# Kernel tuning notes

Hardware: AMD Instinct MI355X
Metric: run time of the kernel (lower is better)

The kernel has to match this reference:

```python
import jax, jax.numpy as jnp
import numpy as np

D_MODEL = 1024
NUM_HEADS = 16
D_K = D_MODEL // NUM_HEADS
NEG = jnp.float32(-1e9)  # finite stand-in for -inf to keep softmax NaN-free on fully masked rows


def setup_inputs() -> dict:
    key = jax.random.key(0)
    ks = jax.random.split(key, 7)
    B, N_q, N_kv = 2, 2048, 2048
    x = jax.random.normal(ks[0], (B, N_q, D_MODEL), dtype=jnp.float32)
    K = jax.random.normal(ks[1], (B, NUM_HEADS, N_kv, D_K), dtype=jnp.float32)
    V = jax.random.normal(ks[2], (B, NUM_HEADS, N_kv, D_K), dtype=jnp.float32)
    # pad masks: True = keep. Ensure first kv position is always valid.
    kv_pad_mask = jax.random.uniform(ks[3], (B, 1, 1, N_kv)) > 0.1
    kv_pad_mask = kv_pad_mask.at[..., 0].set(True)
    q_pad_mask = jax.random.uniform(ks[4], (B, 1, N_q, 1)) > 0.1
    # params (torch Linear, bias=False); stored as [in, out] so y = x @ W
    Wq = jax.random.normal(ks[5], (D_MODEL, D_MODEL), dtype=jnp.float32) / np.sqrt(D_MODEL)
    Wo = jax.random.normal(ks[6], (D_MODEL, D_MODEL), dtype=jnp.float32) / np.sqrt(D_MODEL)
    return {"x": x, "K": K, "V": V, "Wq": Wq, "Wo": Wo,
            "kv_pad_mask": kv_pad_mask, "q_pad_mask": q_pad_mask}


def reference(x, K, V, Wq, Wo, kv_pad_mask, q_pad_mask):
    B, N_q, D = x.shape
    H, d_k = NUM_HEADS, D_K
    # Q projection and split into heads: [B, H, N_q, d_k]
    Q = (x @ Wq).reshape(B, N_q, H, d_k).transpose(0, 2, 1, 3)
    scores = jnp.einsum('bhqd,bhkd->bhqk', Q, K) / np.sqrt(d_k).astype(np.float32)
    keep = q_pad_mask & kv_pad_mask  # broadcast to [B,1,N_q,N_kv]
    scores = jnp.where(keep, scores, NEG)
    probs = jax.nn.softmax(scores, axis=-1)
    attn = jnp.einsum('bhqk,bhkd->bhqd', probs, V)  # [B,H,N_q,d_k]
    attn = attn.transpose(0, 2, 1, 3).reshape(B, N_q, H * d_k)
    return attn @ Wo
```

## Files before the change

kernel.cpp:

```cpp
#include <hip/hip_runtime.h>
#include <hip/hip_bf16.h>
#include <stdint.h>

typedef __hip_bfloat16 bf16;
typedef __attribute__((ext_vector_type(8))) short short8;
typedef __attribute__((ext_vector_type(4))) short s16x4;
typedef __attribute__((ext_vector_type(4))) float floatx4;

#define MFMA16(a, b, c) __builtin_amdgcn_mfma_f32_16x16x32_bf16(a, b, c, 0, 0, 0)

__device__ __forceinline__ void async_lds16(const void* g, void* l) {
  __builtin_amdgcn_global_load_lds((__attribute__((address_space(1))) const void*)g,
                                   (__attribute__((address_space(3))) void*)l, 16, 0, 0);
}

__device__ __forceinline__ unsigned rne2(float a, float b) {
  unsigned ua = __float_as_uint(a), ub = __float_as_uint(b);
  ua = ua + 0x7FFFu + ((ua >> 16) & 1u);
  ub = ub + 0x7FFFu + ((ub >> 16) & 1u);
  return (ua >> 16) | (ub & 0xFFFF0000u);
}

__global__ void prep_masks_k(const int* __restrict__ kv, const int* __restrict__ q,
                             float* __restrict__ kvB, float* __restrict__ qB) {
  int i = blockIdx.x * 256 + threadIdx.x;
  kvB[i] = kv[i] ? 0.0f : -3000.0f;
  qB[i]  = q[i]  ? 0.0f : -3000.0f;
}

__global__ void cvt2_k(const float* __restrict__ a, bf16* __restrict__ da,
                       const float* __restrict__ b, bf16* __restrict__ db) {
  int gid = blockIdx.x;
  const float* s; bf16* d;
  if (gid < 4096) { s = a; d = da; } else { s = b; d = db; gid -= 4096; }
  int i = (gid * 256 + threadIdx.x) * 4;
  float4 v = *(const float4*)(s + i);
  uint2 o = {rne2(v.x, v.y), rne2(v.z, v.w)};
  *(uint2*)(d + i) = o;
}

__global__ __launch_bounds__(256) void cvt_transpose_k(const float* __restrict__ src,
                                                       bf16* __restrict__ dst, int R, int C) {
  __shared__ float tile[64][65];
  int m = blockIdx.z;
  int r0 = blockIdx.x * 64, c0 = blockIdx.y * 64;
  const float* s = src + (size_t)m * R * C;
  bf16* d = dst + (size_t)m * R * C;
  int t = threadIdx.x;
  int tr = t >> 2, tg = t & 3;
#pragma unroll
  for (int k = 0; k < 4; ++k) {
    int col = tg * 16 + k * 4;
    float4 v = *(const float4*)(s + (size_t)(r0 + tr) * C + c0 + col);
    tile[tr][col] = v.x; tile[tr][col + 1] = v.y; tile[tr][col + 2] = v.z; tile[tr][col + 3] = v.w;
  }
  __syncthreads();
  int orow = t >> 2, ch = t & 3;
  bf16* drow = d + (size_t)(c0 + orow) * R + r0;
  uint4 w0, w1;
  w0.x = rne2(tile[ch * 8 + 0][orow], tile[ch * 8 + 1][orow]);
  w0.y = rne2(tile[ch * 8 + 2][orow], tile[ch * 8 + 3][orow]);
  w0.z = rne2(tile[ch * 8 + 4][orow], tile[ch * 8 + 5][orow]);
  w0.w = rne2(tile[ch * 8 + 6][orow], tile[ch * 8 + 7][orow]);
  w1.x = rne2(tile[32 + ch * 8 + 0][orow], tile[32 + ch * 8 + 1][orow]);
  w1.y = rne2(tile[32 + ch * 8 + 2][orow], tile[32 + ch * 8 + 3][orow]);
  w1.z = rne2(tile[32 + ch * 8 + 4][orow], tile[32 + ch * 8 + 5][orow]);
  w1.w = rne2(tile[32 + ch * 8 + 6][orow], tile[32 + ch * 8 + 7][orow]);
  *(uint4*)(drow + ch * 8) = w0;
  *(uint4*)(drow + 32 + ch * 8) = w1;
}

__global__ __launch_bounds__(256) void cvtT_w_k(const float* __restrict__ w0p, bf16* __restrict__ d0,
                                                const float* __restrict__ w1p, bf16* __restrict__ d1) {
  __shared__ float tile[64][65];
  const float* s = blockIdx.z ? w1p : w0p;
  bf16* d = blockIdx.z ? d1 : d0;
  int r0 = blockIdx.x * 64, c0 = blockIdx.y * 64;
  int t = threadIdx.x;
  int tr = t >> 2, tg = t & 3;
#pragma unroll
  for (int k = 0; k < 4; ++k) {
    int col = tg * 16 + k * 4;
    float4 v = *(const float4*)(s + (size_t)(r0 + tr) * 1024 + c0 + col);
    tile[tr][col] = v.x; tile[tr][col + 1] = v.y; tile[tr][col + 2] = v.z; tile[tr][col + 3] = v.w;
  }
  __syncthreads();
  int orow = t >> 2, ch = t & 3;
  bf16* drow = d + (size_t)(c0 + orow) * 1024 + r0;
  uint4 a, b;
  a.x = rne2(tile[ch * 8 + 0][orow], tile[ch * 8 + 1][orow]);
  a.y = rne2(tile[ch * 8 + 2][orow], tile[ch * 8 + 3][orow]);
  a.z = rne2(tile[ch * 8 + 4][orow], tile[ch * 8 + 5][orow]);
  a.w = rne2(tile[ch * 8 + 6][orow], tile[ch * 8 + 7][orow]);
  b.x = rne2(tile[32 + ch * 8 + 0][orow], tile[32 + ch * 8 + 1][orow]);
  b.y = rne2(tile[32 + ch * 8 + 2][orow], tile[32 + ch * 8 + 3][orow]);
  b.z = rne2(tile[32 + ch * 8 + 4][orow], tile[32 + ch * 8 + 5][orow]);
  b.w = rne2(tile[32 + ch * 8 + 6][orow], tile[32 + ch * 8 + 7][orow]);
  *(uint4*)(drow + ch * 8) = a;
  *(uint4*)(drow + 32 + ch * 8) = b;
}

__device__ __forceinline__ void storeC(bf16* C, size_t i, float v) { C[i] = __float2bfloat16(v); }
__device__ __forceinline__ void storeC(float* C, size_t i, float v) { C[i] = v; }

template <typename OT>
__global__ __launch_bounds__(256) void gemm_bt_k(const bf16* __restrict__ A,
                                                 const bf16* __restrict__ BT,
                                                 OT* __restrict__ C,
                                                 int M, int N, int K, float scale) {
  __shared__ __align__(16) bf16 As[128 * 64];
  __shared__ __align__(16) bf16 Bs[64 * 64];
  int tid = threadIdx.x;
  int wave = tid >> 6, lane = tid & 63;
  int quad = lane >> 4, lm = lane & 15;
  int wm = wave >> 1, wn = wave & 1;
  int row0 = blockIdx.y * 128, col0 = blockIdx.x * 64;

  floatx4 acc[4][2];
#pragma unroll
  for (int mt = 0; mt < 4; ++mt)
#pragma unroll
    for (int nt = 0; nt < 2; ++nt) acc[mt][nt] = (floatx4){0.f, 0.f, 0.f, 0.f};

  for (int k0 = 0; k0 < K; k0 += 64) {
    __syncthreads();
#pragma unroll
    for (int ch = 0; ch < 4; ++ch) {
      int e = (wave * 4 + ch) * 512 + lane * 8;
      async_lds16(A + (size_t)(row0 + (e >> 6)) * K + k0 + (e & 63), &As[(wave * 4 + ch) * 512]);
    }
#pragma unroll
    for (int ch = 0; ch < 2; ++ch) {
      int e = (wave * 2 + ch) * 512 + lane * 8;
      async_lds16(BT + (size_t)(col0 + (e >> 6)) * K + k0 + (e & 63), &Bs[(wave * 2 + ch) * 512]);
    }
    __syncthreads();
#pragma unroll
    for (int ks = 0; ks < 64; ks += 32) {
      short8 af[4], bfr[2];
#pragma unroll
      for (int mt = 0; mt < 4; ++mt)
        af[mt] = *(const short8*)&As[(wm * 64 + mt * 16 + lm) * 64 + ks + quad * 8];
#pragma unroll
      for (int nt = 0; nt < 2; ++nt)
        bfr[nt] = *(const short8*)&Bs[(wn * 32 + nt * 16 + lm) * 64 + ks + quad * 8];
#pragma unroll
      for (int mt = 0; mt < 4; ++mt)
#pragma unroll
        for (int nt = 0; nt < 2; ++nt)
          acc[mt][nt] = MFMA16(af[mt], bfr[nt], acc[mt][nt]);
    }
  }
#pragma unroll
  for (int mt = 0; mt < 4; ++mt)
#pragma unroll
    for (int nt = 0; nt < 2; ++nt)
#pragma unroll
      for (int j = 0; j < 4; ++j) {
        int rr = row0 + wm * 64 + mt * 16 + quad * 4 + j;
        int cc = col0 + wn * 32 + nt * 16 + lm;
        storeC(C, (size_t)rr * N + cc, acc[mt][nt][j] * scale);
      }
}

__global__ __launch_bounds__(256, 4) void attn_k(const bf16* __restrict__ Q,
                                                 const bf16* __restrict__ Km,
                                                 const bf16* __restrict__ VT,
                                                 const float* __restrict__ qB,
                                                 const float* __restrict__ kvB,
                                                 bf16* __restrict__ Opart,
                                                 float* __restrict__ lpart) {
  const float TINY = 9.313225746154785e-10f;
  __shared__ __align__(16) bf16 Ks[64 * 64];
  __shared__ __align__(16) bf16 Vs[64 * 64];
  __shared__ __align__(16) float kvBs[512];

  int tid = threadIdx.x;
  int wave = tid >> 6, lane = tid & 63;
  int quad = lane >> 4, lm = lane & 15;
  int qb = blockIdx.x & 15, slice = blockIdx.x >> 4;
  int h = blockIdx.y, b = blockIdx.z;
  int q0 = qb * 128 + wave * 32;
  int kvbeg = slice * 512;

  const bf16* kbase = Km + (size_t)(b * 16 + h) * 2048 * 64;
  const bf16* vbase = VT + (size_t)(b * 16 + h) * 64 * 2048;
  const float* kvBb = kvB + b * 2048;

  if (wave < 2)
    async_lds16(kvBb + kvbeg + wave * 256 + lane * 4, &kvBs[wave * 256]);

  short8 aq[2][2];
  float qbias[2];
#pragma unroll
  for (int g = 0; g < 2; ++g) {
    const bf16* qp = Q + (size_t)(b * 2048 + q0 + g * 16 + lm) * 1024 + h * 64 + quad * 8;
    aq[g][0] = *(const short8*)qp;
    aq[g][1] = *(const short8*)(qp + 32);
    qbias[g] = qB[b * 2048 + q0 + g * 16 + lm];
  }

  short8 ones;
#pragma unroll
  for (int i = 0; i < 8; ++i) ones[i] = (short)0x3F80;

  floatx4 o_acc[2][4];
  floatx4 l_acc[2];
#pragma unroll
  for (int g = 0; g < 2; ++g) {
    l_acc[g] = (floatx4){0.f, 0.f, 0.f, 0.f};
#pragma unroll
    for (int t = 0; t < 4; ++t) o_acc[g][t] = (floatx4){0.f, 0.f, 0.f, 0.f};
  }

  union S8U { short8 s8; s16x4 h[2]; unsigned u[4]; };

  for (int kv0 = kvbeg; kv0 < kvbeg + 512; kv0 += 64) {
    __syncthreads();
#pragma unroll
    for (int c = 0; c < 2; ++c) {
      int o = (wave * 2 + c) * 1024 + lane * 16;
      int r = o >> 7;
      int g16 = (o >> 4) & 7;
      int sc = ((g16 ^ (r & 7)) * 8);
      async_lds16(kbase + (size_t)(kv0 + r) * 64 + sc, &Ks[(wave * 2 + c) * 512]);
      async_lds16(vbase + (size_t)r * 2048 + kv0 + sc, &Vs[(wave * 2 + c) * 512]);
    }
    __syncthreads();

    floatx4 kb4[4];
#pragma unroll
    for (int t = 0; t < 4; ++t)
      kb4[t] = *(const floatx4*)&kvBs[(kv0 - kvbeg) + t * 16 + quad * 4];

    S8U pf[2][2];
#pragma unroll
    for (int t = 0; t < 4; ++t) {
      int R = t * 16 + lm, sw = R & 7;
      short8 kf0 = *(const short8*)&Ks[R * 64 + ((quad ^ sw) * 8)];
      short8 kf1 = *(const short8*)&Ks[R * 64 + (((quad + 4) ^ sw) * 8)];
#pragma unroll
      for (int g = 0; g < 2; ++g) {
        floatx4 z;
#pragma unroll
        for (int j = 0; j < 4; ++j) z[j] = kb4[t][j] + qbias[g];
        z = MFMA16(kf0, aq[g][0], z);
        z = MFMA16(kf1, aq[g][1], z);
        float p0 = __builtin_amdgcn_exp2f(z[0]) + TINY;
        float p1 = __builtin_amdgcn_exp2f(z[1]) + TINY;
        float p2 = __builtin_amdgcn_exp2f(z[2]) + TINY;
        float p3 = __builtin_amdgcn_exp2f(z[3]) + TINY;
        pf[g][t >> 1].u[(t & 1) * 2 + 0] = rne2(p0, p1);
        pf[g][t >> 1].u[(t & 1) * 2 + 1] = rne2(p2, p3);
      }
    }
#pragma unroll
    for (int t = 0; t < 4; ++t) {
      int D = t * 16 + lm, sw = D & 7;
      int hoff = (quad & 1) * 4, qh = quad >> 1;
      S8U vf0, vf1;
      vf0.h[0] = *(const s16x4*)&Vs[D * 64 + (((0 + qh) ^ sw) * 8) + hoff];
      vf0.h[1] = *(const s16x4*)&Vs[D * 64 + (((2 + qh) ^ sw) * 8) + hoff];
      vf1.h[0] = *(const s16x4*)&Vs[D * 64 + (((4 + qh) ^ sw) * 8) + hoff];
      vf1.h[1] = *(const s16x4*)&Vs[D * 64 + (((6 + qh) ^ sw) * 8) + hoff];
#pragma unroll
      for (int g = 0; g < 2; ++g) {
        o_acc[g][t] = MFMA16(vf0.s8, pf[g][0].s8, o_acc[g][t]);
        o_acc[g][t] = MFMA16(vf1.s8, pf[g][1].s8, o_acc[g][t]);
      }
    }
#pragma unroll
    for (int g = 0; g < 2; ++g) {
      l_acc[g] = MFMA16(ones, pf[g][0].s8, l_acc[g]);
      l_acc[g] = MFMA16(ones, pf[g][1].s8, l_acc[g]);
    }
  }
  bf16* Op = Opart + (size_t)slice * (2u * 2048u * 1024u);
#pragma unroll
  for (int g = 0; g < 2; ++g) {
    int q = b * 2048 + q0 + g * 16 + lm;
    bf16* orow = Op + (size_t)q * 1024 + h * 64;
#pragma unroll
    for (int t = 0; t < 4; ++t) {
      uint2 ov = {rne2(o_acc[g][t][0], o_acc[g][t][1]),
                  rne2(o_acc[g][t][2], o_acc[g][t][3])};
      *(uint2*)(orow + t * 16 + quad * 4) = ov;
    }
    if (quad == 0)
      lpart[((size_t)slice * 4096 + (size_t)q) * 16 + h] = l_acc[g][0];
  }
}

__global__ void combine_k(const bf16* __restrict__ Opart, const float* __restrict__ lpart,
                          bf16* __restrict__ out) {
  int i = (blockIdx.x * 256 + threadIdx.x) * 8;
  int bq = i >> 10, h = (i >> 6) & 15;
  float l = lpart[bq * 16 + h] + lpart[65536 + bq * 16 + h] +
            lpart[131072 + bq * 16 + h] + lpart[196608 + bq * 16 + h];
  float rl = 1.0f / l;
  float acc[8];
#pragma unroll
  for (int e = 0; e < 8; ++e) acc[e] = 0.f;
#pragma unroll
  for (int s = 0; s < 4; ++s) {
    uint4 u = *(const uint4*)(Opart + s * 4194304 + i);
    acc[0] += __uint_as_float(u.x << 16); acc[1] += __uint_as_float(u.x & 0xFFFF0000u);
    acc[2] += __uint_as_float(u.y << 16); acc[3] += __uint_as_float(u.y & 0xFFFF0000u);
    acc[4] += __uint_as_float(u.z << 16); acc[5] += __uint_as_float(u.z & 0xFFFF0000u);
    acc[6] += __uint_as_float(u.w << 16); acc[7] += __uint_as_float(u.w & 0xFFFF0000u);
  }
  uint4 o = {rne2(acc[0] * rl, acc[1] * rl), rne2(acc[2] * rl, acc[3] * rl),
             rne2(acc[4] * rl, acc[5] * rl), rne2(acc[6] * rl, acc[7] * rl)};
  *(uint4*)(out + i) = o;
}

extern "C" void kernel_launch(void* const* d_in, const int* in_sizes, int n_in,
                              void* d_out, int out_size, void* d_ws, size_t ws_size,
                              hipStream_t stream) {
  const float* x  = (const float*)d_in[0];
  const float* K  = (const float*)d_in[1];
  const float* V  = (const float*)d_in[2];
  const float* Wq = (const float*)d_in[3];
  const float* Wo = (const float*)d_in[4];
  const int* kvm  = (const int*)d_in[5];
  const int* qm   = (const int*)d_in[6];

  char* w = (char*)d_ws;
  bf16* xb    = (bf16*)(w);
  bf16* attnb = xb;
  bf16* Qb    = (bf16*)(w + (8u << 20));
  bf16* Kb    = (bf16*)(w + (16u << 20));
  bf16* VTb   = (bf16*)(w + (24u << 20));
  bf16* WqT   = (bf16*)(w + (32u << 20));
  bf16* WoT   = (bf16*)(w + (34u << 20));
  float* qB   = (float*)(w + (36u << 20));
  float* kvB  = (float*)(w + (36u << 20) + 16384);
  bf16* Opart = (bf16*)(w + (40u << 20));
  float* lpart = (float*)(w + (72u << 20));

  const float SCL2 = 0.18033688011112042f;

  prep_masks_k<<<16, 256, 0, stream>>>(kvm, qm, kvB, qB);
  cvt2_k<<<8192, 256, 0, stream>>>(x, xb, K, Kb);
  cvtT_w_k<<<dim3(16, 16, 2), 256, 0, stream>>>(Wq, WqT, Wo, WoT);
  cvt_transpose_k<<<dim3(32, 1, 32), 256, 0, stream>>>(V, VTb, 2048, 64);

  gemm_bt_k<bf16><<<dim3(16, 32), 256, 0, stream>>>(xb, WqT, Qb, 4096, 1024, 1024, SCL2);
  attn_k<<<dim3(64, 16, 2), 256, 0, stream>>>(Qb, Kb, VTb, qB, kvB, Opart, lpart);
  combine_k<<<2048, 256, 0, stream>>>(Opart, lpart, attnb);
  gemm_bt_k<float><<<dim3(16, 32), 256, 0, stream>>>(attnb, WoT, (float*)d_out, 4096, 1024, 1024, 1.0f);
}
```

Baseline: 216.1 us.

## Merge prep kernels, drop split-KV combine, shrink GEMM tiles with swizzled LDS

```diff
diff --git a/kernel.cpp b/kernel.cpp
--- a/kernel.cpp
+++ b/kernel.cpp
@@ -21,83 +21,64 @@
   return (ua >> 16) | (ub & 0xFFFF0000u);
 }
 
-__global__ void prep_masks_k(const int* __restrict__ kv, const int* __restrict__ q,
-                             float* __restrict__ kvB, float* __restrict__ qB) {
-  int i = blockIdx.x * 256 + threadIdx.x;
-  kvB[i] = kv[i] ? 0.0f : -3000.0f;
-  qB[i]  = q[i]  ? 0.0f : -3000.0f;
-}
-
-__global__ void cvt2_k(const float* __restrict__ a, bf16* __restrict__ da,
-                       const float* __restrict__ b, bf16* __restrict__ db) {
-  int gid = blockIdx.x;
-  const float* s; bf16* d;
-  if (gid < 4096) { s = a; d = da; } else { s = b; d = db; gid -= 4096; }
-  int i = (gid * 256 + threadIdx.x) * 4;
-  float4 v = *(const float4*)(s + i);
-  uint2 o = {rne2(v.x, v.y), rne2(v.z, v.w)};
-  *(uint2*)(d + i) = o;
-}
-
-__global__ __launch_bounds__(256) void cvt_transpose_k(const float* __restrict__ src,
-                                                       bf16* __restrict__ dst, int R, int C) {
+__global__ __launch_bounds__(256) void prep_k(const float* __restrict__ x, bf16* __restrict__ xb,
+                                              const float* __restrict__ Kf, bf16* __restrict__ Kb,
+                                              const float* __restrict__ Wq, bf16* __restrict__ WqT,
+                                              const float* __restrict__ Wo, bf16* __restrict__ WoT,
+                                              const float* __restrict__ V, bf16* __restrict__ VTb,
+                                              const int* __restrict__ kvm, const int* __restrict__ qm,
+                                              float* __restrict__ kvB, float* __restrict__ qB) {
   __shared__ float tile[64][65];
-  int m = blockIdx.z;
-  int r0 = blockIdx.x * 64, c0 = blockIdx.y * 64;
-  const float* s = src + (size_t)m * R * C;
-  bf16* d = dst + (size_t)m * R * C;
-  int t = threadIdx.x;
-  int tr = t >> 2, tg = t & 3;
-#pragma unroll
-  for (int k = 0; k < 4; ++k) {
-    int col = tg * 16 + k * 4;
-    float4 v = *(const float4*)(s + (size_t)(r0 + tr) * C + c0 + col);
-    tile[tr][col] = v.x; tile[tr][col + 1] = v.y; tile[tr][col + 2] = v.z; tile[tr][col + 3] = v.w;
-  }
-  __syncthreads();
-  int orow = t >> 2, ch = t & 3;
-  bf16* drow = d + (size_t)(c0 + orow) * R + r0;
-  uint4 w0, w1;
-  w0.x = rne2(tile[ch * 8 + 0][orow], tile[ch * 8 + 1][orow]);
-  w0.y = rne2(tile[ch * 8 + 2][orow], tile[ch * 8 + 3][orow]);
-  w0.z = rne2(tile[ch * 8 + 4][orow], tile[ch * 8 + 5][orow]);
-  w0.w = rne2(tile[ch * 8 + 6][orow], tile[ch * 8 + 7][orow]);
-  w1.x = rne2(tile[32 + ch * 8 + 0][orow], tile[32 + ch * 8 + 1][orow]);
-  w1.y = rne2(tile[32 + ch * 8 + 2][orow], tile[32 + ch * 8 + 3][orow]);
-  w1.z = rne2(tile[32 + ch * 8 + 4][orow], tile[32 + ch * 8 + 5][orow]);
-  w1.w = rne2(tile[32 + ch * 8 + 6][orow], tile[32 + ch * 8 + 7][orow]);
-  *(uint4*)(drow + ch * 8) = w0;
-  *(uint4*)(drow + 32 + ch * 8) = w1;
-}
-
-__global__ __launch_bounds__(256) void cvtT_w_k(const float* __restrict__ w0p, bf16* __restrict__ d0,
-                                                const float* __restrict__ w1p, bf16* __restrict__ d1) {
-  __shared__ float tile[64][65];
-  const float* s = blockIdx.z ? w1p : w0p;
-  bf16* d = blockIdx.z ? d1 : d0;
-  int r0 = blockIdx.x * 64, c0 = blockIdx.y * 64;
-  int t = threadIdx.x;
-  int tr = t >> 2, tg = t & 3;
-#pragma unroll
-  for (int k = 0; k < 4; ++k) {
-    int col = tg * 16 + k * 4;
-    float4 v = *(const float4*)(s + (size_t)(r0 + tr) * 1024 + c0 + col);
-    tile[tr][col] = v.x; tile[tr][col + 1] = v.y; tile[tr][col + 2] = v.z; tile[tr][col + 3] = v.w;
-  }
-  __syncthreads();
-  int orow = t >> 2, ch = t & 3;
-  bf16* drow = d + (size_t)(c0 + orow) * 1024 + r0;
-  uint4 a, b;
-  a.x = rne2(tile[ch * 8 + 0][orow], tile[ch * 8 + 1][orow]);
-  a.y = rne2(tile[ch * 8 + 2][orow], tile[ch * 8 + 3][orow]);
-  a.z = rne2(tile[ch * 8 + 4][orow], tile[ch * 8 + 5][orow]);
-  a.w = rne2(tile[ch * 8 + 6][orow], tile[ch * 8 + 7][orow]);
-  b.x = rne2(tile[32 + ch * 8 + 0][orow], tile[32 + ch * 8 + 1][orow]);
-  b.y = rne2(tile[32 + ch * 8 + 2][orow], tile[32 + ch * 8 + 3][orow]);
-  b.z = rne2(tile[32 + ch * 8 + 4][orow], tile[32 + ch * 8 + 5][orow]);
-  b.w = rne2(tile[32 + ch * 8 + 6][orow], tile[32 + ch * 8 + 7][orow]);
-  *(uint4*)(drow + ch * 8) = a;
-  *(uint4*)(drow + 32 + ch * 8) = b;
+  int bid = blockIdx.x, tid = threadIdx.x;
+  if (bid < 8192) {
+    const float* s; bf16* d; int g = bid;
+    if (g < 4096) { s = x; d = xb; } else { s = Kf; d = Kb; g -= 4096; }
+    int i = (g * 256 + tid) * 4;
+    float4 v = *(const float4*)(s + i);
+    uint2 o = {rne2(v.x, v.y), rne2(v.z, v.w)};
+    *(uint2*)(d + i) = o;
+    return;
+  }
+  if (bid < 9744 - 16) {
+    const float* s; bf16* d; int r0, c0, R, C;
+    if (bid < 8704) {
+      int idx = bid - 8192;
+      s = (idx >> 8) ? Wo : Wq; d = (idx >> 8) ? WoT : WqT;
+      int rem = idx & 255;
+      r0 = (rem & 15) * 64; c0 = (rem >> 4) * 64; R = 1024; C = 1024;
+    } else {
+      int idx = bid - 8704;
+      int m = idx >> 5;
+      s = V + (size_t)m * 2048 * 64; d = VTb + (size_t)m * 2048 * 64;
+      r0 = (idx & 31) * 64; c0 = 0; R = 2048; C = 64;
+    }
+    int tr = tid >> 2, tg = tid & 3;
+#pragma unroll
+    for (int k = 0; k < 4; ++k) {
+      int col = tg * 16 + k * 4;
+      float4 v = *(const float4*)(s + (size_t)(r0 + tr) * C + c0 + col);
+      tile[tr][col] = v.x; tile[tr][col + 1] = v.y;
+      tile[tr][col + 2] = v.z; tile[tr][col + 3] = v.w;
+    }
+    __syncthreads();
+    int orow = tid >> 2, ch = tid & 3;
+    bf16* drow = d + (size_t)(c0 + orow) * R + r0;
+    uint4 w0, w1;
+    w0.x = rne2(tile[ch * 8 + 0][orow], tile[ch * 8 + 1][orow]);
+    w0.y = rne2(tile[ch * 8 + 2][orow], tile[ch * 8 + 3][orow]);
+    w0.z = rne2(tile[ch * 8 + 4][orow], tile[ch * 8 + 5][orow]);
+    w0.w = rne2(tile[ch * 8 + 6][orow], tile[ch * 8 + 7][orow]);
+    w1.x = rne2(tile[32 + ch * 8 + 0][orow], tile[32 + ch * 8 + 1][orow]);
+    w1.y = rne2(tile[32 + ch * 8 + 2][orow], tile[32 + ch * 8 + 3][orow]);
+    w1.z = rne2(tile[32 + ch * 8 + 4][orow], tile[32 + ch * 8 + 5][orow]);
+    w1.w = rne2(tile[32 + ch * 8 + 6][orow], tile[32 + ch * 8 + 7][orow]);
+    *(uint4*)(drow + ch * 8) = w0;
+    *(uint4*)(drow + 32 + ch * 8) = w1;
+    return;
+  }
+  int i = (bid - (9744 - 16)) * 256 + tid;
+  kvB[i] = kvm[i] ? 0.0f : -3000.0f;
+  qB[i]  = qm[i]  ? 0.0f : -3000.0f;
 }
 
 __device__ __forceinline__ void storeC(bf16* C, size_t i, float v) { C[i] = __float2bfloat16(v); }
@@ -108,56 +89,65 @@
                                                  const bf16* __restrict__ BT,
                                                  OT* __restrict__ C,
                                                  int M, int N, int K, float scale) {
-  __shared__ __align__(16) bf16 As[128 * 64];
+  __shared__ __align__(16) bf16 As[64 * 64];
   __shared__ __align__(16) bf16 Bs[64 * 64];
   int tid = threadIdx.x;
   int wave = tid >> 6, lane = tid & 63;
   int quad = lane >> 4, lm = lane & 15;
   int wm = wave >> 1, wn = wave & 1;
-  int row0 = blockIdx.y * 128, col0 = blockIdx.x * 64;
-
-  floatx4 acc[4][2];
-#pragma unroll
-  for (int mt = 0; mt < 4; ++mt)
+  int row0 = blockIdx.y * 64, col0 = blockIdx.x * 64;
+
+  floatx4 acc[2][2];
+#pragma unroll
+  for (int mt = 0; mt < 2; ++mt)
 #pragma unroll
     for (int nt = 0; nt < 2; ++nt) acc[mt][nt] = (floatx4){0.f, 0.f, 0.f, 0.f};
 
   for (int k0 = 0; k0 < K; k0 += 64) {
     __syncthreads();
-#pragma unroll
-    for (int ch = 0; ch < 4; ++ch) {
-      int e = (wave * 4 + ch) * 512 + lane * 8;
-      async_lds16(A + (size_t)(row0 + (e >> 6)) * K + k0 + (e & 63), &As[(wave * 4 + ch) * 512]);
-    }
 #pragma unroll
     for (int ch = 0; ch < 2; ++ch) {
       int e = (wave * 2 + ch) * 512 + lane * 8;
-      async_lds16(BT + (size_t)(col0 + (e >> 6)) * K + k0 + (e & 63), &Bs[(wave * 2 + ch) * 512]);
-    }
-    __syncthreads();
+      int r = e >> 6, c16 = (e & 63) >> 3;
+      int sc = (c16 ^ (r & 7)) * 8;
+      async_lds16(A + (size_t)(row0 + r) * K + k0 + sc, &As[(wave * 2 + ch) * 512]);
+    }
+#pragma unroll
+    for (int ch = 0; ch < 2; ++ch) {
+      int e = (wave * 2 + ch) * 512 + lane * 8;
+      int r = e >> 6, c16 = (e & 63) >> 3;
+      int sc = (c16 ^ (r & 7)) * 8;
+      async_lds16(BT + (size_t)(col0 + r) * K + k0 + sc, &Bs[(wave * 2 + ch) * 512]);
+    }
+    __syncthreads();
+    int sw = lm & 7;
 #pragma unroll
     for (int ks = 0; ks < 64; ks += 32) {
-      short8 af[4], bfr[2];
-#pragma unroll
-      for (int mt = 0; mt < 4; ++mt)
-        af[mt] = *(const short8*)&As[(wm * 64 + mt * 16 + lm) * 64 + ks + quad * 8];
-#pragma unroll
-      for (int nt = 0; nt < 2; ++nt)
-        bfr[nt] = *(const short8*)&Bs[(wn * 32 + nt * 16 + lm) * 64 + ks + quad * 8];
-#pragma unroll
-      for (int mt = 0; mt < 4; ++mt)
+      short8 af[2], bfr[2];
+#pragma unroll
+      for (int mt = 0; mt < 2; ++mt) {
+        int R = wm * 32 + mt * 16 + lm;
+        af[mt] = *(const short8*)&As[R * 64 + ((((ks >> 3) + quad) ^ sw) * 8)];
+      }
+#pragma unroll
+      for (int nt = 0; nt < 2; ++nt) {
+        int R = wn * 32 + nt * 16 + lm;
+        bfr[nt] = *(const short8*)&Bs[R * 64 + ((((ks >> 3) + quad) ^ sw) * 8)];
+      }
+#pragma unroll
+      for (int mt = 0; mt < 2; ++mt)
 #pragma unroll
         for (int nt = 0; nt < 2; ++nt)
           acc[mt][nt] = MFMA16(af[mt], bfr[nt], acc[mt][nt]);
     }
   }
 #pragma unroll
-  for (int mt = 0; mt < 4; ++mt)
+  for (int mt = 0; mt < 2; ++mt)
 #pragma unroll
     for (int nt = 0; nt < 2; ++nt)
 #pragma unroll
       for (int j = 0; j < 4; ++j) {
-        int rr = row0 + wm * 64 + mt * 16 + quad * 4 + j;
+        int rr = row0 + wm * 32 + mt * 16 + quad * 4 + j;
         int cc = col0 + wn * 32 + nt * 16 + lm;
         storeC(C, (size_t)rr * N + cc, acc[mt][nt][j] * scale);
       }
@@ -168,54 +158,47 @@
                                                  const bf16* __restrict__ VT,
                                                  const float* __restrict__ qB,
                                                  const float* __restrict__ kvB,
-                                                 bf16* __restrict__ Opart,
-                                                 float* __restrict__ lpart) {
+                                                 bf16* __restrict__ O) {
   const float TINY = 9.313225746154785e-10f;
   __shared__ __align__(16) bf16 Ks[64 * 64];
   __shared__ __align__(16) bf16 Vs[64 * 64];
-  __shared__ __align__(16) float kvBs[512];
+  __shared__ __align__(16) float kvBs[2048];
 
   int tid = threadIdx.x;
   int wave = tid >> 6, lane = tid & 63;
   int quad = lane >> 4, lm = lane & 15;
-  int qb = blockIdx.x & 15, slice = blockIdx.x >> 4;
-  int h = blockIdx.y, b = blockIdx.z;
-  int q0 = qb * 128 + wave * 32;
-  int kvbeg = slice * 512;
+  int qb = blockIdx.x, h = blockIdx.y, b = blockIdx.z;
+  int q0 = qb * 64 + wave * 16;
 
   const bf16* kbase = Km + (size_t)(b * 16 + h) * 2048 * 64;
   const bf16* vbase = VT + (size_t)(b * 16 + h) * 64 * 2048;
   const float* kvBb = kvB + b * 2048;
 
-  if (wave < 2)
-    async_lds16(kvBb + kvbeg + wave * 256 + lane * 4, &kvBs[wave * 256]);
-
-  short8 aq[2][2];
-  float qbias[2];
-#pragma unroll
-  for (int g = 0; g < 2; ++g) {
-    const bf16* qp = Q + (size_t)(b * 2048 + q0 + g * 16 + lm) * 1024 + h * 64 + quad * 8;
-    aq[g][0] = *(const short8*)qp;
-    aq[g][1] = *(const short8*)(qp + 32);
-    qbias[g] = qB[b * 2048 + q0 + g * 16 + lm];
+#pragma unroll
+  for (int c = 0; c < 2; ++c)
+    async_lds16(kvBb + (wave * 2 + c) * 256 + lane * 4, &kvBs[(wave * 2 + c) * 256]);
+
+  short8 aq0, aq1;
+  float qbias;
+  {
+    const bf16* qp = Q + (size_t)(b * 2048 + q0 + lm) * 1024 + h * 64 + quad * 8;
+    aq0 = *(const short8*)qp;
+    aq1 = *(const short8*)(qp + 32);
+    qbias = qB[b * 2048 + q0 + lm];
   }
 
   short8 ones;
 #pragma unroll
   for (int i = 0; i < 8; ++i) ones[i] = (short)0x3F80;
 
-  floatx4 o_acc[2][4];
-  floatx4 l_acc[2];
-#pragma unroll
-  for (int g = 0; g < 2; ++g) {
-    l_acc[g] = (floatx4){0.f, 0.f, 0.f, 0.f};
-#pragma unroll
-    for (int t = 0; t < 4; ++t) o_acc[g][t] = (floatx4){0.f, 0.f, 0.f, 0.f};
-  }
+  floatx4 o_acc[4];
+  floatx4 l_acc = (floatx4){0.f, 0.f, 0.f, 0.f};
+#pragma unroll
+  for (int t = 0; t < 4; ++t) o_acc[t] = (floatx4){0.f, 0.f, 0.f, 0.f};
 
   union S8U { short8 s8; s16x4 h[2]; unsigned u[4]; };
 
-  for (int kv0 = kvbeg; kv0 < kvbeg + 512; kv0 += 64) {
+  for (int kv0 = 0; kv0 < 2048; kv0 += 64) {
     __syncthreads();
 #pragma unroll
     for (int c = 0; c < 2; ++c) {
@@ -228,90 +211,47 @@
     }
     __syncthreads();
 
-    floatx4 kb4[4];
-#pragma unroll
-    for (int t = 0; t < 4; ++t)
-      kb4[t] = *(const floatx4*)&kvBs[(kv0 - kvbeg) + t * 16 + quad * 4];
-
-    S8U pf[2][2];
+    S8U pf[2];
 #pragma unroll
     for (int t = 0; t < 4; ++t) {
-      int R = t * 16 + lm, sw = R & 7;
+      int R = t * 16 + lm, sw = lm & 7;
       short8 kf0 = *(const short8*)&Ks[R * 64 + ((quad ^ sw) * 8)];
       short8 kf1 = *(const short8*)&Ks[R * 64 + (((quad + 4) ^ sw) * 8)];
-#pragma unroll
-      for (int g = 0; g < 2; ++g) {
-        floatx4 z;
-#pragma unroll
-        for (int j = 0; j < 4; ++j) z[j] = kb4[t][j] + qbias[g];
-        z = MFMA16(kf0, aq[g][0], z);
-        z = MFMA16(kf1, aq[g][1], z);
-        float p0 = __builtin_amdgcn_exp2f(z[0]) + TINY;
-        float p1 = __builtin_amdgcn_exp2f(z[1]) + TINY;
-        float p2 = __builtin_amdgcn_exp2f(z[2]) + TINY;
-        float p3 = __builtin_amdgcn_exp2f(z[3]) + TINY;
-        pf[g][t >> 1].u[(t & 1) * 2 + 0] = rne2(p0, p1);
-        pf[g][t >> 1].u[(t & 1) * 2 + 1] = rne2(p2, p3);
-      }
+      floatx4 z = *(const floatx4*)&kvBs[kv0 + t * 16 + quad * 4];
+#pragma unroll
+      for (int j = 0; j < 4; ++j) z[j] += qbias;
+      z = MFMA16(kf0, aq0, z);
+      z = MFMA16(kf1, aq1, z);
+      float p0 = __builtin_amdgcn_exp2f(z[0]) + TINY;
+      float p1 = __builtin_amdgcn_exp2f(z[1]) + TINY;
+      float p2 = __builtin_amdgcn_exp2f(z[2]) + TINY;
+      float p3 = __builtin_amdgcn_exp2f(z[3]) + TINY;
+      pf[t >> 1].u[(t & 1) * 2 + 0] = rne2(p0, p1);
+      pf[t >> 1].u[(t & 1) * 2 + 1] = rne2(p2, p3);
     }
 #pragma unroll
     for (int t = 0; t < 4; ++t) {
-      int D = t * 16 + lm, sw = D & 7;
+      int D = t * 16 + lm, sw = lm & 7;
       int hoff = (quad & 1) * 4, qh = quad >> 1;
       S8U vf0, vf1;
       vf0.h[0] = *(const s16x4*)&Vs[D * 64 + (((0 + qh) ^ sw) * 8) + hoff];
       vf0.h[1] = *(const s16x4*)&Vs[D * 64 + (((2 + qh) ^ sw) * 8) + hoff];
       vf1.h[0] = *(const s16x4*)&Vs[D * 64 + (((4 + qh) ^ sw) * 8) + hoff];
       vf1.h[1] = *(const s16x4*)&Vs[D * 64 + (((6 + qh) ^ sw) * 8) + hoff];
-#pragma unroll
-      for (int g = 0; g < 2; ++g) {
-        o_acc[g][t] = MFMA16(vf0.s8, pf[g][0].s8, o_acc[g][t]);
-        o_acc[g][t] = MFMA16(vf1.s8, pf[g][1].s8, o_acc[g][t]);
-      }
-    }
-#pragma unroll
-    for (int g = 0; g < 2; ++g) {
-      l_acc[g] = MFMA16(ones, pf[g][0].s8, l_acc[g]);
-      l_acc[g] = MFMA16(ones, pf[g][1].s8, l_acc[g]);
-    }
-  }
-  bf16* Op = Opart + (size_t)slice * (2u * 2048u * 1024u);
-#pragma unroll
-  for (int g = 0; g < 2; ++g) {
-    int q = b * 2048 + q0 + g * 16 + lm;
-    bf16* orow = Op + (size_t)q * 1024 + h * 64;
-#pragma unroll
-    for (int t = 0; t < 4; ++t) {
-      uint2 ov = {rne2(o_acc[g][t][0], o_acc[g][t][1]),
-                  rne2(o_acc[g][t][2], o_acc[g][t][3])};
-      *(uint2*)(orow + t * 16 + quad * 4) = ov;
-    }
-    if (quad == 0)
-      lpart[((size_t)slice * 4096 + (size_t)q) * 16 + h] = l_acc[g][0];
-  }
-}
-
-__global__ void combine_k(const bf16* __restrict__ Opart, const float* __restrict__ lpart,
-                          bf16* __restrict__ out) {
-  int i = (blockIdx.x * 256 + threadIdx.x) * 8;
-  int bq = i >> 10, h = (i >> 6) & 15;
-  float l = lpart[bq * 16 + h] + lpart[65536 + bq * 16 + h] +
-            lpart[131072 + bq * 16 + h] + lpart[196608 + bq * 16 + h];
-  float rl = 1.0f / l;
-  float acc[8];
-#pragma unroll
-  for (int e = 0; e < 8; ++e) acc[e] = 0.f;
-#pragma unroll
-  for (int s = 0; s < 4; ++s) {
-    uint4 u = *(const uint4*)(Opart + s * 4194304 + i);
-    acc[0] += __uint_as_float(u.x << 16); acc[1] += __uint_as_float(u.x & 0xFFFF0000u);
-    acc[2] += __uint_as_float(u.y << 16); acc[3] += __uint_as_float(u.y & 0xFFFF0000u);
-    acc[4] += __uint_as_float(u.z << 16); acc[5] += __uint_as_float(u.z & 0xFFFF0000u);
-    acc[6] += __uint_as_float(u.w << 16); acc[7] += __uint_as_float(u.w & 0xFFFF0000u);
-  }
-  uint4 o = {rne2(acc[0] * rl, acc[1] * rl), rne2(acc[2] * rl, acc[3] * rl),
-             rne2(acc[4] * rl, acc[5] * rl), rne2(acc[6] * rl, acc[7] * rl)};
-  *(uint4*)(out + i) = o;
+      o_acc[t] = MFMA16(vf0.s8, pf[0].s8, o_acc[t]);
+      o_acc[t] = MFMA16(vf1.s8, pf[1].s8, o_acc[t]);
+    }
+    l_acc = MFMA16(ones, pf[0].s8, l_acc);
+    l_acc = MFMA16(ones, pf[1].s8, l_acc);
+  }
+  float rl = 1.0f / l_acc[0];
+  bf16* orow = O + (size_t)(b * 2048 + q0 + lm) * 1024 + h * 64;
+#pragma unroll
+  for (int t = 0; t < 4; ++t) {
+    uint2 ov = {rne2(o_acc[t][0] * rl, o_acc[t][1] * rl),
+                rne2(o_acc[t][2] * rl, o_acc[t][3] * rl)};
+    *(uint2*)(orow + t * 16 + quad * 4) = ov;
+  }
 }
 
 extern "C" void kernel_launch(void* const* d_in, const int* in_sizes, int n_in,
@@ -335,18 +275,11 @@
   bf16* WoT   = (bf16*)(w + (34u << 20));
   float* qB   = (float*)(w + (36u << 20));
   float* kvB  = (float*)(w + (36u << 20) + 16384);
-  bf16* Opart = (bf16*)(w + (40u << 20));
-  float* lpart = (float*)(w + (72u << 20));
 
   const float SCL2 = 0.18033688011112042f;
 
-  prep_masks_k<<<16, 256, 0, stream>>>(kvm, qm, kvB, qB);
-  cvt2_k<<<8192, 256, 0, stream>>>(x, xb, K, Kb);
-  cvtT_w_k<<<dim3(16, 16, 2), 256, 0, stream>>>(Wq, WqT, Wo, WoT);
-  cvt_transpose_k<<<dim3(32, 1, 32), 256, 0, stream>>>(V, VTb, 2048, 64);
-
-  gemm_bt_k<bf16><<<dim3(16, 32), 256, 0, stream>>>(xb, WqT, Qb, 4096, 1024, 1024, SCL2);
-  attn_k<<<dim3(64, 16, 2), 256, 0, stream>>>(Qb, Kb, VTb, qB, kvB, Opart, lpart);
-  combine_k<<<2048, 256, 0, stream>>>(Opart, lpart, attnb);
-  gemm_bt_k<float><<<dim3(16, 32), 256, 0, stream>>>(attnb, WoT, (float*)d_out, 4096, 1024, 1024, 1.0f);
-}
+  prep_k<<<9744, 256, 0, stream>>>(x, xb, K, Kb, Wq, WqT, Wo, WoT, V, VTb, kvm, qm, kvB, qB);
+  gemm_bt_k<bf16><<<dim3(16, 64), 256, 0, stream>>>(xb, WqT, Qb, 4096, 1024, 1024, SCL2);
+  attn_k<<<dim3(32, 16, 2), 256, 0, stream>>>(Qb, Kb, VTb, qB, kvB, attnb);
+  gemm_bt_k<float><<<dim3(16, 64), 256, 0, stream>>>(attnb, WoT, (float*)d_out, 4096, 1024, 1024, 1.0f);
+}
```

New measurement: 204.6 us. 5.3% less time.
